# Performance work log

Measured on AMD Instinct MI355X. Metric: run time of the kernel, lower is better.

## Reference

```python
import jax, jax.numpy as jnp
import numpy as np

N_NODES = 4096
N_EDGES = 32768
IN_FEAT = 256
OUT_FEAT = 128
HID = 64
IN_HEAD = 64
OUT_HEAD = 5
NEG_SLOPE = 0.2
EPS = 1e-16


def setup_inputs() -> dict:
    key = jax.random.key(0)
    ks = jax.random.split(key, 12)
    x = jax.random.normal(ks[0], (N_NODES, IN_FEAT), dtype=jnp.float32)
    src = jax.random.randint(ks[1], (N_EDGES,), 0, N_NODES)
    dst = jax.random.randint(ks[2], (N_EDGES,), 0, N_NODES)
    edge_index = jnp.stack([src, dst]).astype(jnp.int64)
    s1 = 1.0 / np.sqrt(IN_FEAT)
    s2 = 1.0 / np.sqrt(HID * IN_HEAD)
    W1 = jax.random.normal(ks[3], (IN_FEAT, IN_HEAD * HID), dtype=jnp.float32) * s1
    att_src1 = jax.random.normal(ks[4], (IN_HEAD, HID), dtype=jnp.float32) * 0.1
    att_dst1 = jax.random.normal(ks[5], (IN_HEAD, HID), dtype=jnp.float32) * 0.1
    b1 = jnp.zeros((IN_HEAD * HID,), dtype=jnp.float32)
    W2 = jax.random.normal(ks[6], (IN_HEAD * HID, OUT_HEAD * OUT_FEAT), dtype=jnp.float32) * s2
    att_src2 = jax.random.normal(ks[7], (OUT_HEAD, OUT_FEAT), dtype=jnp.float32) * 0.1
    att_dst2 = jax.random.normal(ks[8], (OUT_HEAD, OUT_FEAT), dtype=jnp.float32) * 0.1
    b2 = jnp.zeros((OUT_FEAT,), dtype=jnp.float32)
    return {"x": x, "edge_index": edge_index, "W1": W1, "att_src1": att_src1,
            "att_dst1": att_dst1, "b1": b1, "W2": W2, "att_src2": att_src2,
            "att_dst2": att_dst2, "b2": b2}


def _gat_conv(x, W, att_src, att_dst, bias, src, dst, heads, out_c, concat):
    # x: [N, F_in]; returns [N, heads*out_c] (concat) or [N, out_c] (mean)
    n = x.shape[0]
    h = (x @ W).reshape(n, heads, out_c)                       # [N,H,C]
    a_src = jnp.sum(h * att_src, axis=-1)                      # [N,H]
    a_dst = jnp.sum(h * att_dst, axis=-1)                      # [N,H]
    e = jax.nn.leaky_relu(a_src[src] + a_dst[dst], NEG_SLOPE)  # [E,H]
    # segment softmax over edges grouped by destination node (PyG softmax)
    m = jax.ops.segment_max(e, dst, num_segments=n)            # [N,H]
    ex = jnp.exp(e - m[dst])
    denom = jax.ops.segment_sum(ex, dst, num_segments=n)       # [N,H]
    alpha = ex / (denom[dst] + EPS)                            # [E,H]
    out = jax.ops.segment_sum(alpha[:, :, None] * h[src], dst, num_segments=n)  # [N,H,C]
    out = out.reshape(n, heads * out_c) if concat else out.mean(axis=1)
    return out + bias


def reference(x, edge_index, W1, att_src1, att_dst1, b1, W2, att_src2, att_dst2, b2):
    n = x.shape[0]
    # PyG GATConv default: add self loops
    loop = jnp.arange(n, dtype=edge_index.dtype)
    src = jnp.concatenate([edge_index[0], loop])
    dst = jnp.concatenate([edge_index[1], loop])
    # dropout layers are identity in eval mode
    h = _gat_conv(x, W1, att_src1, att_dst1, b1, src, dst, IN_HEAD, HID, True)
    h = jax.nn.elu(h)
    h = _gat_conv(h, W2, att_src2, att_dst2, b2, src, dst, OUT_HEAD, OUT_FEAT, False)
    s = jnp.mean(h, axis=0)
    return jnp.tanh(s)
```

## Files before the change

### kernel.cpp

```cpp
#include <hip/hip_runtime.h>
#include <hip/hip_bf16.h>

#define N_NODES 4096
#define NE      32768
#define E_TOT   (NE + N_NODES)
#define IN_FEAT 256
#define HID     64
#define IN_HEAD 64
#define F1      4096
#define OUT_HEAD 5
#define OUT_FEAT 128
#define F2      640
#define NEG_SLOPE 0.2f
#define EPS_A   1e-16f

typedef __bf16 bf16;
typedef bf16 bf16x8 __attribute__((ext_vector_type(8)));
typedef bf16 bf16x4 __attribute__((ext_vector_type(4)));
typedef float f32x4 __attribute__((ext_vector_type(4)));

__device__ inline void async_cp16(bf16* lds, const bf16* g) {
    __builtin_amdgcn_global_load_lds(
        (const __attribute__((address_space(1))) unsigned int*)g,
        (__attribute__((address_space(3))) unsigned int*)lds, 16, 0, 0);
}

template <typename TC>
__device__ __forceinline__ void gemm_body(
    const bf16* __restrict__ A, const bf16* __restrict__ BT, TC* __restrict__ Cz,
    int m0, int n0, int kbeg, int kchunk, int Ncols, int Kdim,
    bf16 (*As)[64], bf16 (*Bs)[64], int tid) {
    const int wave = tid >> 6, lane = tid & 63;
    const int quad = lane >> 4, lr = lane & 15;
    const int wm = (wave >> 1) * 64;
    const int wn = (wave & 1) * 64;
    const int srow = lane >> 3;
    const int scol = ((lane & 7) ^ srow) * 8;
    const int xk = lr & 7;

    f32x4 acc[4][4] = {};

    for (int kk = 0; kk < kchunk; kk += 64) {
        int k0 = kbeg + kk;
#pragma unroll
        for (int c = 0; c < 4; ++c) {
            int r = wave * 32 + c * 8;
            async_cp16(&As[r][0], A + (size_t)(m0 + r + srow) * Kdim + k0 + scol);
            async_cp16(&Bs[r][0], BT + (size_t)(n0 + r + srow) * Kdim + k0 + scol);
        }
        __syncthreads();

#pragma unroll
        for (int ks = 0; ks < 2; ++ks) {
            int ch = ((ks * 4 + quad) ^ xk) * 8;
            bf16x8 af[4], bfr[4];
#pragma unroll
            for (int mt = 0; mt < 4; ++mt)
                af[mt] = *(const bf16x8*)(&As[wm + mt * 16 + lr][ch]);
#pragma unroll
            for (int nt = 0; nt < 4; ++nt)
                bfr[nt] = *(const bf16x8*)(&Bs[wn + nt * 16 + lr][ch]);
#pragma unroll
            for (int mt = 0; mt < 4; ++mt)
#pragma unroll
                for (int nt = 0; nt < 4; ++nt)
                    acc[mt][nt] = __builtin_amdgcn_mfma_f32_16x16x32_bf16(
                        af[mt], bfr[nt], acc[mt][nt], 0, 0, 0);
        }
        __syncthreads();
    }

#pragma unroll
    for (int mt = 0; mt < 4; ++mt)
#pragma unroll
        for (int nt = 0; nt < 4; ++nt) {
            int row0 = m0 + wm + mt * 16 + quad * 4;
            int col = n0 + wn + nt * 16 + lr;
#pragma unroll
            for (int r = 0; r < 4; ++r)
                Cz[(size_t)(row0 + r) * Ncols + col] = (TC)acc[mt][nt][r];
        }
}

#define PB_H   144
#define PB_X   512
#define PB_W1  1024
#define PB_W2  2560
__global__ __launch_bounds__(256)
void phaseA_kernel(const int* __restrict__ edst, int* __restrict__ counts,
                   const float* __restrict__ x, bf16* __restrict__ xb,
                   const float* __restrict__ W1, bf16* __restrict__ W1T,
                   const float* __restrict__ W2, bf16* __restrict__ W2T,
                   const float* __restrict__ as1, const float* __restrict__ ad1,
                   bf16* __restrict__ w1s, bf16* __restrict__ w1d) {
    __shared__ float tile[32][33];
    int b0 = blockIdx.x, t = threadIdx.x;
    if (b0 < PB_H) {
        int e = b0 * 256 + t;
        if (e < E_TOT) {
            int d = (e < NE) ? edst[e] : (e - NE);
            atomicAdd(&counts[d], 1);
        }
        return;
    }
    int b = b0 - PB_H;
    if (b < PB_X) {
        int i = b * 256 + t;
        f32x4 a = *(const f32x4*)(x + (size_t)i * 8);
        f32x4 c = *(const f32x4*)(x + (size_t)i * 8 + 4);
        bf16x8 r;
        r[0] = (bf16)a[0]; r[1] = (bf16)a[1]; r[2] = (bf16)a[2]; r[3] = (bf16)a[3];
        r[4] = (bf16)c[0]; r[5] = (bf16)c[1]; r[6] = (bf16)c[2]; r[7] = (bf16)c[3];
        *(bf16x8*)(xb + (size_t)i * 8) = r;
    } else if (b < PB_X + PB_W1 + PB_W2) {
        const float* S; bf16* D; int R, C, gx, gy;
        if (b < PB_X + PB_W1) {
            int bb = b - PB_X;
            S = W1; D = W1T; R = IN_FEAT; C = F1;
            gx = bb % (F1 / 32); gy = bb / (F1 / 32);
        } else {
            int bb = b - PB_X - PB_W1;
            S = W2; D = W2T; R = F1; C = F2;
            gx = bb % (F2 / 32); gy = bb / (F2 / 32);
        }
        int tx = t & 31, ty = t >> 5;
        int c0 = gx * 32, r0 = gy * 32;
#pragma unroll
        for (int i = 0; i < 4; ++i)
            tile[ty + i * 8][tx] = S[(size_t)(r0 + ty + i * 8) * C + c0 + tx];
        __syncthreads();
#pragma unroll
        for (int i = 0; i < 4; ++i)
            D[(size_t)(c0 + ty + i * 8) * R + r0 + tx] = (bf16)tile[tx][ty + i * 8];
    } else {
        int id = (b - PB_X - PB_W1 - PB_W2) * 256 + t;
        int k = id >> 6, h = id & 63;
        const float* wrow = W1 + (size_t)k * F1 + h * HID;
        const float* a1 = as1 + h * HID;
        const float* a2 = ad1 + h * HID;
        float s = 0.f, d = 0.f;
#pragma unroll 8
        for (int c = 0; c < HID; ++c) {
            float w = wrow[c];
            s += w * a1[c];
            d += w * a2[c];
        }
        w1s[id] = (bf16)s;
        w1d[id] = (bf16)d;
    }
}

__global__ void scan_kernel(const int* __restrict__ counts,
                            int* __restrict__ row_start, int* __restrict__ cursor) {
    __shared__ int part[256];
    __shared__ int pre[257];
    int t = threadIdx.x;
    int base = t * 16;
    int local[16];
    int s = 0;
#pragma unroll
    for (int i = 0; i < 16; ++i) { local[i] = s; s += counts[base + i]; }
    part[t] = s;
    __syncthreads();
    if (t == 0) {
        int r = 0;
        for (int i = 0; i < 256; ++i) { pre[i] = r; r += part[i]; }
        pre[256] = r;
    }
    __syncthreads();
    int off = pre[t];
#pragma unroll
    for (int i = 0; i < 16; ++i) {
        int v = off + local[i];
        row_start[base + i] = v;
        cursor[base + i] = v;
    }
    if (t == 0) row_start[N_NODES] = pre[256];
}

#define PS_S   144
__global__ __launch_bounds__(256)
void phaseS_kernel(const int* __restrict__ edst, int* cursor, int* __restrict__ elist,
                   const float* __restrict__ x,
                   const bf16* __restrict__ w1s, const bf16* __restrict__ w1d,
                   float* __restrict__ a_src, float* __restrict__ a_dst) {
    int b = blockIdx.x, t = threadIdx.x;
    if (b < PS_S) {
        int e = b * 256 + t;
        if (e < E_TOT) {
            int d = (e < NE) ? edst[e] : (e - NE);
            int slot = atomicAdd(&cursor[d], 1);
            elist[slot] = e;
        }
    } else {
        int nblk = b - PS_S;
        int wave = t >> 6, lane = t & 63;
        int n = nblk * 4 + wave;
        const float* xr = x + (size_t)n * IN_FEAT;
        float s = 0.f, d = 0.f;
        for (int k0 = 0; k0 < IN_FEAT; k0 += 4) {
            f32x4 xv = *(const f32x4*)(xr + k0);
#pragma unroll
            for (int j = 0; j < 4; ++j) {
                float xs = xv[j];
                s += xs * (float)w1s[(k0 + j) * IN_HEAD + lane];
                d += xs * (float)w1d[(k0 + j) * IN_HEAD + lane];
            }
        }
        a_src[n * IN_HEAD + lane] = s;
        a_dst[n * IN_HEAD + lane] = d;
    }
}

__global__ __launch_bounds__(256)
void gemm1_kernel(const bf16* __restrict__ A, const bf16* __restrict__ BT,
                  bf16* __restrict__ C) {
    __shared__ bf16 As[128][64];
    __shared__ bf16 Bs[128][64];
    int bid = blockIdx.x;
    int xx = bid & 7, q = bid >> 3;
    int mb = xx * 4 + (q >> 5);
    int nb = q & 31;
    gemm_body<bf16>(A, BT, C, mb * 128, nb * 128, 0, IN_FEAT,
                    F1, IN_FEAT, As, Bs, threadIdx.x);
}

__global__ __launch_bounds__(64)
void agg1_kernel(const int* __restrict__ es, const int* __restrict__ row_start,
                 const int* __restrict__ elist,
                 const float* __restrict__ a_src, const float* __restrict__ a_dst,
                 const bf16* __restrict__ H1, const float* __restrict__ b1,
                 bf16* __restrict__ h_elu) {
    int bid = blockIdx.x;
    int c = bid & 7;
    int d = bid >> 3;
    int lane = threadIdx.x;
    int gh = c * 8 + (lane >> 3);
    int sub = lane & 7;
    int beg = row_start[d], deg = row_start[d + 1] - beg;
    float adst = a_dst[d * IN_HEAD + gh];

    float m = -1e30f, den = 0.f;
    for (int i = sub; i < deg; i += 8) {
        int e = elist[beg + i];
        int s = (e < NE) ? es[e] : d;
        float l = a_src[s * IN_HEAD + gh] + adst;
        l = l > 0.f ? l : NEG_SLOPE * l;
        if (l > m) { den = den * __expf(m - l) + 1.f; m = l; }
        else den += __expf(l - m);
    }
#pragma unroll
    for (int o = 1; o <= 4; o <<= 1) {
        float mo = __shfl_xor(m, o);
        float dno = __shfl_xor(den, o);
        float mn = fmaxf(m, mo);
        den = den * __expf(m - mn) + dno * __expf(mo - mn);
        m = mn;
    }
    float dinv = 1.f / (den + EPS_A);

    int fbase = c * 512 + lane * 8;
    float acc[8] = {};
#pragma unroll 2
    for (int i = 0; i < deg; ++i) {
        int e = elist[beg + i];
        int s = (e < NE) ? es[e] : d;
        float l = a_src[s * IN_HEAD + gh] + adst;
        l = l > 0.f ? l : NEG_SLOPE * l;
        float alpha = __expf(l - m) * dinv;
        bf16x8 v = *(const bf16x8*)(H1 + (size_t)s * F1 + fbase);
#pragma unroll
        for (int j = 0; j < 8; ++j) acc[j] += alpha * (float)v[j];
    }

    bf16x8 o;
#pragma unroll
    for (int j = 0; j < 8; ++j) {
        float v = acc[j] + b1[fbase + j];
        o[j] = (bf16)(v > 0.f ? v : (__expf(v) - 1.f));
    }
    *(bf16x8*)(h_elu + (size_t)d * F1 + fbase) = o;
}

__global__ __launch_bounds__(256)
void gemm2_kernel(const bf16* __restrict__ A, const bf16* __restrict__ BT,
                  bf16* __restrict__ C) {
    __shared__ bf16 As[128][64];
    __shared__ bf16 Bs[128][64];
    int bid = blockIdx.x;
    int xx = bid & 7, q = bid >> 3;
    int gp = q / 5, nb = q - gp * 5;
    int g = gp * 8 + xx;
    int mb = g >> 2, zb = g & 3;
    const int kchunk = F1 / 4;
    gemm_body<bf16>(A, BT, C + (size_t)zb * N_NODES * F2,
                    mb * 128, nb * 128, zb * kchunk, kchunk,
                    F2, F1, As, Bs, threadIdx.x);
}

__global__ __launch_bounds__(192)
void fold2_kernel(const bf16* __restrict__ Hp,
                  const float* __restrict__ as2, const float* __restrict__ ad2,
                  float* __restrict__ H2,
                  float* __restrict__ a_src, float* __restrict__ a_dst) {
    int n = blockIdx.x, t = threadIdx.x;
    if (t >= 160) return;
    int h = t >> 5;
    f32x4 sum = {};
#pragma unroll
    for (int z = 0; z < 4; ++z) {
        bf16x4 v = *(const bf16x4*)(Hp + (size_t)z * N_NODES * F2 + (size_t)n * F2 + t * 4);
        sum[0] += (float)v[0]; sum[1] += (float)v[1];
        sum[2] += (float)v[2]; sum[3] += (float)v[3];
    }
    *(f32x4*)(H2 + (size_t)n * F2 + t * 4) = sum;
    f32x4 ws = *(const f32x4*)(as2 + t * 4);
    f32x4 wd = *(const f32x4*)(ad2 + t * 4);
    float s = sum[0] * ws[0] + sum[1] * ws[1] + sum[2] * ws[2] + sum[3] * ws[3];
    float d = sum[0] * wd[0] + sum[1] * wd[1] + sum[2] * wd[2] + sum[3] * wd[3];
#pragma unroll
    for (int o = 1; o <= 16; o <<= 1) {
        s += __shfl_xor(s, o);
        d += __shfl_xor(d, o);
    }
    if ((t & 31) == 0) {
        a_src[n * OUT_HEAD + h] = s;
        a_dst[n * OUT_HEAD + h] = d;
    }
}

__global__ void statsbeta2_kernel(const int* __restrict__ es,
                                  const int* __restrict__ row_start,
                                  const int* __restrict__ elist,
                                  const float* __restrict__ a_src,
                                  const float* __restrict__ a_dst,
                                  float* __restrict__ beta) {
    int id = blockIdx.x * 256 + threadIdx.x;
    if (id >= N_NODES * OUT_HEAD) return;
    int d = id / OUT_HEAD, h = id - d * OUT_HEAD;
    int beg = row_start[d], deg = row_start[d + 1] - beg;
    float adst = a_dst[id];
    float m = -1e30f, den = 0.f;
    for (int i = 0; i < deg; ++i) {
        int e = elist[beg + i];
        int s = (e < NE) ? es[e] : d;
        float l = a_src[s * OUT_HEAD + h] + adst;
        l = l > 0.f ? l : NEG_SLOPE * l;
        if (l > m) { den = den * __expf(m - l) + 1.f; m = l; }
        else den += __expf(l - m);
    }
    float dinv = 1.f / (den + EPS_A);
    for (int i = 0; i < deg; ++i) {
        int e = elist[beg + i];
        int s = (e < NE) ? es[e] : d;
        float l = a_src[s * OUT_HEAD + h] + adst;
        l = l > 0.f ? l : NEG_SLOPE * l;
        float alpha = __expf(l - m) * dinv;
        atomicAdd(&beta[s * OUT_HEAD + h], alpha);
    }
}

__global__ __launch_bounds__(256)
void wsum_kernel(const float* __restrict__ H2, const float* __restrict__ beta,
                 float* __restrict__ acc_out, int* __restrict__ done_ctr,
                 const float* __restrict__ b2, float* __restrict__ out) {
    __shared__ float buf[F2];
    __shared__ int lflag;
    int t = threadIdx.x;
    int n0 = blockIdx.x * 32;
    int h = t >> 5;
    float a0 = 0.f, a1 = 0.f, a2 = 0.f, a3 = 0.f;
    if (t < 160) {
        for (int i = 0; i < 32; ++i) {
            int s = n0 + i;
            float bh = beta[s * OUT_HEAD + h];
            f32x4 v = *(const f32x4*)(H2 + (size_t)s * F2 + t * 4);
            a0 += bh * v[0]; a1 += bh * v[1];
            a2 += bh * v[2]; a3 += bh * v[3];
        }
        buf[t * 4 + 0] = a0; buf[t * 4 + 1] = a1;
        buf[t * 4 + 2] = a2; buf[t * 4 + 3] = a3;
    }
    __syncthreads();
    if (t < OUT_FEAT) {
        float s = 0.f;
#pragma unroll
        for (int hh = 0; hh < OUT_HEAD; ++hh) s += buf[hh * OUT_FEAT + t];
        atomicAdd(&acc_out[(blockIdx.x & 7) * OUT_FEAT + t], s);
    }
    __threadfence();
    __syncthreads();
    if (t == 0) lflag = (atomicAdd(done_ctr, 1) == (N_NODES / 32) - 1);
    __syncthreads();
    if (lflag && t < OUT_FEAT) {
        float tot = 0.f;
#pragma unroll
        for (int k = 0; k < 8; ++k)
            tot += __hip_atomic_load(&acc_out[k * OUT_FEAT + t],
                                     __ATOMIC_RELAXED, __HIP_MEMORY_SCOPE_AGENT);
        out[t] = tanhf(tot * (1.f / (OUT_HEAD * (float)N_NODES)) + b2[t]);
    }
}

extern "C" void kernel_launch(void* const* d_in, const int* in_sizes, int n_in,
                              void* d_out, int out_size, void* d_ws, size_t ws_size,
                              hipStream_t stream) {
    const float* x        = (const float*)d_in[0];
    const int*   ei       = (const int*)d_in[1];
    const float* W1       = (const float*)d_in[2];
    const float* att_src1 = (const float*)d_in[3];
    const float* att_dst1 = (const float*)d_in[4];
    const float* b1       = (const float*)d_in[5];
    const float* W2       = (const float*)d_in[6];
    const float* att_src2 = (const float*)d_in[7];
    const float* att_dst2 = (const float*)d_in[8];
    const float* b2       = (const float*)d_in[9];
    float* out = (float*)d_out;

    const int* esrc = ei;
    const int* edst = ei + NE;

    char* p = (char*)d_ws;
    auto bump = [&](size_t bytes) {
        void* r = (void*)p;
        p += (bytes + 255) & ~(size_t)255;
        return r;
    };
    bf16*  H1     = (bf16*)bump((size_t)N_NODES * F1 * 2);
    bf16*  h_elu  = (bf16*)bump((size_t)N_NODES * F1 * 2);
    float* H2     = (float*)bump((size_t)N_NODES * F2 * 4);
    bf16*  xb     = (bf16*)bump((size_t)N_NODES * IN_FEAT * 2);
    bf16*  W1T    = (bf16*)bump((size_t)F1 * IN_FEAT * 2);
    bf16*  W2T    = (bf16*)bump((size_t)F2 * F1 * 2);
    bf16*  w1s    = (bf16*)bump((size_t)IN_FEAT * IN_HEAD * 2);
    bf16*  w1d    = (bf16*)bump((size_t)IN_FEAT * IN_HEAD * 2);
    float* a_src1 = (float*)bump((size_t)N_NODES * IN_HEAD * 4);
    float* a_dst1 = (float*)bump((size_t)N_NODES * IN_HEAD * 4);
    float* a_src2 = (float*)bump((size_t)N_NODES * OUT_HEAD * 4);
    float* a_dst2 = (float*)bump((size_t)N_NODES * OUT_HEAD * 4);
    int*   row_start = (int*)bump((N_NODES + 1) * 4);
    int*   cursor = (int*)bump(N_NODES * 4);
    int*   elist  = (int*)bump(E_TOT * 4);
    size_t zbytes = N_NODES * 4 + N_NODES * OUT_HEAD * 4 + 8 * OUT_FEAT * 4 + 256;
    int*   counts = (int*)bump(zbytes);
    float* beta    = (float*)((char*)counts + N_NODES * 4);
    float* acc_out = beta + N_NODES * OUT_HEAD;
    int*   done_ctr = (int*)(acc_out + 8 * OUT_FEAT);
    bf16* Hp = H1;

    hipMemsetAsync(counts, 0, zbytes, stream);

    phaseA_kernel<<<PB_H + PB_X + PB_W1 + PB_W2 + 64, 256, 0, stream>>>(
        edst, counts, x, xb, W1, W1T, W2, W2T, att_src1, att_dst1, w1s, w1d);
    scan_kernel<<<1, 256, 0, stream>>>(counts, row_start, cursor);
    phaseS_kernel<<<PS_S + N_NODES / 4, 256, 0, stream>>>(
        edst, cursor, elist, x, w1s, w1d, a_src1, a_dst1);
    gemm1_kernel<<<1024, 256, 0, stream>>>(xb, W1T, H1);
    agg1_kernel<<<N_NODES * 8, 64, 0, stream>>>(
        esrc, row_start, elist, a_src1, a_dst1, H1, b1, h_elu);
    gemm2_kernel<<<640, 256, 0, stream>>>(h_elu, W2T, Hp);
    fold2_kernel<<<N_NODES, 192, 0, stream>>>(
        Hp, att_src2, att_dst2, H2, a_src2, a_dst2);
    statsbeta2_kernel<<<(N_NODES * OUT_HEAD + 255) / 256, 256, 0, stream>>>(
        esrc, row_start, elist, a_src2, a_dst2, beta);
    wsum_kernel<<<N_NODES / 32, 256, 0, stream>>>(
        H2, beta, acc_out, done_ctr, b2, out);
}
```

Before: 264.6 us.

## Raise gemm2 split-K to 8 and split beta scatter into edge-parallel kernel

The second GEMM's split-K goes from 4 to 8 chunks, launching 1280 blocks instead of 640 and writing partials to a dedicated buffer, so the fold kernel now sums 8 partials. The serial per-destination second loop that atomically scattered alpha values is moved into a separate edge-parallel kernel that reads stored max and inverse-denominator values. The aim is more parallelism in the GEMM and in the beta accumulation. The cost is doubled partial-sum traffic, an extra buffer and one more kernel launch.

```diff
diff --git a/kernel.cpp b/kernel.cpp
--- a/kernel.cpp
+++ b/kernel.cpp
@@ -13,6 +13,7 @@
 #define F2      640
 #define NEG_SLOPE 0.2f
 #define EPS_A   1e-16f
+#define ZSPLIT  8
 
 typedef __bf16 bf16;
 typedef bf16 bf16x8 __attribute__((ext_vector_type(8)));
@@ -290,9 +291,8 @@
     int bid = blockIdx.x;
     int xx = bid & 7, q = bid >> 3;
     int gp = q / 5, nb = q - gp * 5;
-    int g = gp * 8 + xx;
-    int mb = g >> 2, zb = g & 3;
-    const int kchunk = F1 / 4;
+    int mb = gp, zb = xx;
+    const int kchunk = F1 / ZSPLIT;
     gemm_body<bf16>(A, BT, C + (size_t)zb * N_NODES * F2,
                     mb * 128, nb * 128, zb * kchunk, kchunk,
                     F2, F1, As, Bs, threadIdx.x);
@@ -308,7 +308,7 @@
     int h = t >> 5;
     f32x4 sum = {};
 #pragma unroll
-    for (int z = 0; z < 4; ++z) {
+    for (int z = 0; z < ZSPLIT; ++z) {
         bf16x4 v = *(const bf16x4*)(Hp + (size_t)z * N_NODES * F2 + (size_t)n * F2 + t * 4);
         sum[0] += (float)v[0]; sum[1] += (float)v[1];
         sum[2] += (float)v[2]; sum[3] += (float)v[3];
@@ -329,12 +329,12 @@
     }
 }
 
-__global__ void statsbeta2_kernel(const int* __restrict__ es,
-                                  const int* __restrict__ row_start,
-                                  const int* __restrict__ elist,
-                                  const float* __restrict__ a_src,
-                                  const float* __restrict__ a_dst,
-                                  float* __restrict__ beta) {
+__global__ void stats2_kernel(const int* __restrict__ es,
+                              const int* __restrict__ row_start,
+                              const int* __restrict__ elist,
+                              const float* __restrict__ a_src,
+                              const float* __restrict__ a_dst,
+                              float* __restrict__ m2, float* __restrict__ dinv2) {
     int id = blockIdx.x * 256 + threadIdx.x;
     if (id >= N_NODES * OUT_HEAD) return;
     int d = id / OUT_HEAD, h = id - d * OUT_HEAD;
@@ -349,15 +349,23 @@
         if (l > m) { den = den * __expf(m - l) + 1.f; m = l; }
         else den += __expf(l - m);
     }
-    float dinv = 1.f / (den + EPS_A);
-    for (int i = 0; i < deg; ++i) {
-        int e = elist[beg + i];
-        int s = (e < NE) ? es[e] : d;
-        float l = a_src[s * OUT_HEAD + h] + adst;
-        l = l > 0.f ? l : NEG_SLOPE * l;
-        float alpha = __expf(l - m) * dinv;
-        atomicAdd(&beta[s * OUT_HEAD + h], alpha);
-    }
+    m2[id] = m;
+    dinv2[id] = 1.f / (den + EPS_A);
+}
+
+__global__ void beta_kernel(const int* __restrict__ es, const int* __restrict__ ed,
+                            const float* __restrict__ a_src, const float* __restrict__ a_dst,
+                            const float* __restrict__ m2, const float* __restrict__ dinv2,
+                            float* __restrict__ beta) {
+    int id = blockIdx.x * 256 + threadIdx.x;
+    if (id >= E_TOT * OUT_HEAD) return;
+    int e = id / OUT_HEAD, h = id - e * OUT_HEAD;
+    int s = (e < NE) ? es[e] : (e - NE);
+    int d = (e < NE) ? ed[e] : (e - NE);
+    float l = a_src[s * OUT_HEAD + h] + a_dst[d * OUT_HEAD + h];
+    l = l > 0.f ? l : NEG_SLOPE * l;
+    float alpha = __expf(l - m2[d * OUT_HEAD + h]) * dinv2[d * OUT_HEAD + h];
+    atomicAdd(&beta[s * OUT_HEAD + h], alpha);
 }
 
 __global__ __launch_bounds__(256)
@@ -429,6 +437,7 @@
     bf16*  H1     = (bf16*)bump((size_t)N_NODES * F1 * 2);
     bf16*  h_elu  = (bf16*)bump((size_t)N_NODES * F1 * 2);
     float* H2     = (float*)bump((size_t)N_NODES * F2 * 4);
+    bf16*  Hp     = (bf16*)bump((size_t)ZSPLIT * N_NODES * F2 * 2);
     bf16*  xb     = (bf16*)bump((size_t)N_NODES * IN_FEAT * 2);
     bf16*  W1T    = (bf16*)bump((size_t)F1 * IN_FEAT * 2);
     bf16*  W2T    = (bf16*)bump((size_t)F2 * F1 * 2);
@@ -438,6 +447,8 @@
     float* a_dst1 = (float*)bump((size_t)N_NODES * IN_HEAD * 4);
     float* a_src2 = (float*)bump((size_t)N_NODES * OUT_HEAD * 4);
     float* a_dst2 = (float*)bump((size_t)N_NODES * OUT_HEAD * 4);
+    float* m2     = (float*)bump((size_t)N_NODES * OUT_HEAD * 4);
+    float* dinv2  = (float*)bump((size_t)N_NODES * OUT_HEAD * 4);
     int*   row_start = (int*)bump((N_NODES + 1) * 4);
     int*   cursor = (int*)bump(N_NODES * 4);
     int*   elist  = (int*)bump(E_TOT * 4);
@@ -446,7 +457,6 @@
     float* beta    = (float*)((char*)counts + N_NODES * 4);
     float* acc_out = beta + N_NODES * OUT_HEAD;
     int*   done_ctr = (int*)(acc_out + 8 * OUT_FEAT);
-    bf16* Hp = H1;
 
     hipMemsetAsync(counts, 0, zbytes, stream);
 
@@ -458,11 +468,13 @@
     gemm1_kernel<<<1024, 256, 0, stream>>>(xb, W1T, H1);
     agg1_kernel<<<N_NODES * 8, 64, 0, stream>>>(
         esrc, row_start, elist, a_src1, a_dst1, H1, b1, h_elu);
-    gemm2_kernel<<<640, 256, 0, stream>>>(h_elu, W2T, Hp);
+    gemm2_kernel<<<ZSPLIT * 160, 256, 0, stream>>>(h_elu, W2T, Hp);
     fold2_kernel<<<N_NODES, 192, 0, stream>>>(
         Hp, att_src2, att_dst2, H2, a_src2, a_dst2);
-    statsbeta2_kernel<<<(N_NODES * OUT_HEAD + 255) / 256, 256, 0, stream>>>(
-        esrc, row_start, elist, a_src2, a_dst2, beta);
+    stats2_kernel<<<(N_NODES * OUT_HEAD + 255) / 256, 256, 0, stream>>>(
+        esrc, row_start, elist, a_src2, a_dst2, m2, dinv2);
+    beta_kernel<<<(E_TOT * OUT_HEAD + 255) / 256, 256, 0, stream>>>(
+        esrc, edst, a_src2, a_dst2, m2, dinv2, beta);
     wsum_kernel<<<N_NODES / 32, 256, 0, stream>>>(
         H2, beta, acc_out, done_ctr, b2, out);
 }
```

Result: faster. 251.8 us (-4.8%).
